# Optimization experiments

Measured on AMD Instinct MI355X. Metric: run time of the kernel, lower is better.

The kernel has to match this reference:

```python
import jax, jax.numpy as jnp
import numpy as np

MEMBRANE_DECAY = 0.95
REFRACTORY_PERIOD = 2.0


def setup_inputs() -> dict:
    key = jax.random.key(0)
    k0, k1, k2, k3 = jax.random.split(key, 4)
    B, S, I, H, O = 32, 1024, 256, 512, 256
    x = jax.random.normal(k0, (B, S, I), dtype=jnp.float32)
    input_weights = jax.random.normal(k1, (I, H), dtype=jnp.float32) * 0.1
    lateral_weights = jax.random.normal(k2, (H, H), dtype=jnp.float32) * 0.3
    output_weights = jax.random.normal(k3, (H, O), dtype=jnp.float32) * 0.1
    thresholds = jnp.ones((H,), dtype=jnp.float32)  # spike_threshold = 1.0
    return {"x": x, "input_weights": input_weights,
            "lateral_weights": lateral_weights,
            "output_weights": output_weights, "thresholds": thresholds}


def reference(x, input_weights, lateral_weights, output_weights, thresholds):
    # x: [B, S, I]. Precompute input currents for all timesteps: [B, S, H]
    inp_cur = jnp.einsum('bsi,ih->bsh', x, input_weights)
    B, S, H = inp_cur.shape
    dtype = x.dtype

    def step(carry, ic):
        mp, refrac, prev_spikes = carry  # each [B, H]
        # lateral feedback from previous timestep's spikes (zeros at t=0)
        lateral = prev_spikes @ lateral_weights
        mp = MEMBRANE_DECAY * mp + ic - lateral
        mp = jnp.where(refrac > 0, jnp.zeros((), dtype), mp)
        refrac = jnp.maximum(refrac - 1.0, 0.0)
        spikes = (mp >= thresholds).astype(dtype)
        mp = jnp.where(spikes > 0, jnp.zeros((), dtype), mp)
        refrac = jnp.where(spikes > 0, jnp.asarray(REFRACTORY_PERIOD, dtype), refrac)
        return (mp, refrac, spikes), spikes

    init = (jnp.zeros((B, H), dtype), jnp.zeros((B, H), dtype), jnp.zeros((B, H), dtype))
    _, spikes_seq = jax.lax.scan(step, init, jnp.swapaxes(inp_cur, 0, 1))  # [S, B, H]
    # output currents per timestep -> [B, S, O]
    return jnp.einsum('sbh,ho->bso', spikes_seq, output_weights)
```

## Files before the change

### kernel.cpp

```cpp
#include <hip/hip_runtime.h>
#include <stdint.h>


#define BB 32
#define SS 1024
#define II 256
#define HH 512
#define OO 256
#define NSPL 8
#define MAGICK 0x5A5A5A5A5A5A5A5AULL

#define TM 64
#define TN 64
#define TK 16

__global__ __launch_bounds__(256) void ic_gemm_f64(const float* __restrict__ x,
                                                   const float* __restrict__ win,
                                                   double* __restrict__ ic) {
    __shared__ float As[TK][TM + 4];
    __shared__ float Bs[TK][TN];
    const int tid = threadIdx.x;
    const int m0 = blockIdx.x * TM;
    const int n0 = blockIdx.y * TN;
    const int tx = tid & 15;
    const int ty = tid >> 4;

    double acc[4][4];
#pragma unroll
    for (int i = 0; i < 4; ++i)
#pragma unroll
        for (int j = 0; j < 4; ++j) acc[i][j] = 0.0;

    const int lr = tid >> 2;
    const int lq = tid & 3;
    const int br = tid >> 4;
    const int bq = tid & 15;

    for (int k0 = 0; k0 < II; k0 += TK) {
        float4 av = *(const float4*)(x + (size_t)(m0 + lr) * II + k0 + lq * 4);
        float4 bv = *(const float4*)(win + (size_t)(k0 + br) * HH + n0 + bq * 4);
        As[lq * 4 + 0][lr] = av.x;
        As[lq * 4 + 1][lr] = av.y;
        As[lq * 4 + 2][lr] = av.z;
        As[lq * 4 + 3][lr] = av.w;
        *(float4*)(&Bs[br][bq * 4]) = bv;
        __syncthreads();
#pragma unroll
        for (int kk = 0; kk < TK; ++kk) {
            float4 a = *(const float4*)(&As[kk][ty * 4]);
            float4 b = *(const float4*)(&Bs[kk][tx * 4]);
            const double a0 = (double)a.x, a1 = (double)a.y, a2 = (double)a.z, a3 = (double)a.w;
            const double b0 = (double)b.x, b1 = (double)b.y, b2 = (double)b.z, b3 = (double)b.w;
            acc[0][0] += a0 * b0; acc[0][1] += a0 * b1; acc[0][2] += a0 * b2; acc[0][3] += a0 * b3;
            acc[1][0] += a1 * b0; acc[1][1] += a1 * b1; acc[1][2] += a1 * b2; acc[1][3] += a1 * b3;
            acc[2][0] += a2 * b0; acc[2][1] += a2 * b1; acc[2][2] += a2 * b2; acc[2][3] += a2 * b3;
            acc[3][0] += a3 * b0; acc[3][1] += a3 * b1; acc[3][2] += a3 * b2; acc[3][3] += a3 * b3;
        }
        __syncthreads();
    }

#pragma unroll
    for (int i = 0; i < 4; ++i) {
        double* row = ic + (size_t)(m0 + ty * 4 + i) * HH + n0 + tx * 4;
#pragma unroll
        for (int j = 0; j < 4; ++j) row[j] = acc[i][j];
    }
}

__global__ __launch_bounds__(256) void snn_scan8(const double* __restrict__ ic,
                                                 const float* __restrict__ wlat,
                                                 const float* __restrict__ thr,
                                                 uint64_t* __restrict__ xq) {
    __shared__ int s_act[2][560];
    __shared__ int s_nact[2];
    __shared__ double s_part[16][68];
    __shared__ uint64_t s_m8[8];

    const int tid = threadIdx.x;
    const int bid = blockIdx.x;
    const int b = bid & 31;
    const int j = bid >> 5;
    const int ch = tid >> 4;
    const int qd = tid & 15;
    const int sw = (qd >> 2) & 3;

    const double* icb = ic + (size_t)b * SS * HH + (j << 6);
    uint64_t* xqb = xq + ((size_t)b * SS << 4);
    const char* wb = (const char*)wlat + (j << 8) + (qd << 4);

    const bool owner = (tid < 64);
    double mp = 0.0, th = 0.0, icv = 0.0;
    int refrac = 0, rsw = 0;
    if (owner) {
        th = (double)thr[(j << 6) + tid];
        rsw = tid ^ ((tid >> 4) & 3);
        icv = icb[tid];
    }
    if (tid == 0) { s_nact[0] = 0; s_nact[1] = 0; }
    for (int i = tid; i < 560; i += 256) { s_act[0][i] = 0; s_act[1][i] = 0; }
    __syncthreads();

    int cur = 0;
    for (int t = 0; t < SS; ++t) {
        const int nxt = cur ^ 1;

        const int n = s_nact[cur];
        const int* act = s_act[cur];
        const int kcnt = (n > ch) ? ((n - ch + 15) >> 4) : 0;

        double ac0 = 0.0, ac1 = 0.0, ac2 = 0.0, ac3 = 0.0;
        {
            int idx = ch;
            float4 f0 = *(const float4*)(wb + act[idx]);
            float4 f1 = *(const float4*)(wb + act[idx + 16]);
            for (int k = 0; k < kcnt; ++k) {
                float4 f2 = *(const float4*)(wb + act[idx + 32]);
                ac0 += (double)f0.x;
                ac1 += (double)f0.y;
                ac2 += (double)f0.z;
                ac3 += (double)f0.w;
                f0 = f1; f1 = f2; idx += 16;
            }
        }
        {
            const int pb = qd << 2;
            s_part[ch][(pb + 0) ^ sw] = ac0;
            s_part[ch][(pb + 1) ^ sw] = ac1;
            s_part[ch][(pb + 2) ^ sw] = ac2;
            s_part[ch][(pb + 3) ^ sw] = ac3;
        }
        __syncthreads();

        if (owner) {
            double l0 = 0.0, l1 = 0.0, l2 = 0.0, l3 = 0.0;
#pragma unroll
            for (int c = 0; c < 16; c += 4) {
                l0 += s_part[c + 0][rsw];
                l1 += s_part[c + 1][rsw];
                l2 += s_part[c + 2][rsw];
                l3 += s_part[c + 3][rsw];
            }
            const double lat = (l0 + l1) + (l2 + l3);
            mp = 0.95 * mp + icv - lat;
            if (refrac > 0) mp = 0.0;
            refrac = (refrac > 0) ? (refrac - 1) : 0;
            const bool spike = (mp >= th);
            if (spike) { mp = 0.0; refrac = 2; }

            const uint64_t bm = __ballot(spike);
            if (tid == 0) {
                uint64_t* cell = xqb + ((size_t)t << 4) + (j << 1);
                __hip_atomic_store(cell, bm, __ATOMIC_RELAXED,
                                   __HIP_MEMORY_SCOPE_AGENT);
                __hip_atomic_store(cell + 1, bm ^ MAGICK, __ATOMIC_RELAXED,
                                   __HIP_MEMORY_SCOPE_AGENT);
                s_m8[j] = bm;
            }

            if (tid < 16) {
                const int w = tid & 7;
                if (w != j) {
                    uint64_t* rc = xqb + ((size_t)t << 4) + (w << 1) + (tid >> 3);
                    long guard = 0;
                    uint64_t v;
                    for (;;) {
                        v = __hip_atomic_load(rc, __ATOMIC_RELAXED,
                                              __HIP_MEMORY_SCOPE_AGENT);
                        const uint64_t pv = __shfl(v, tid ^ 8, 64);
                        if ((v ^ pv) == MAGICK) break;
                        if (++guard > (1L << 31)) break;
                    }
                    if (tid < 8) s_m8[w] = v;
                }
            }
            icv = icb[(size_t)(t < SS - 1 ? t + 1 : t) * HH + tid];
        } else {
            for (int i = tid - 64; i < 560; i += 192) s_act[nxt][i] = 0;
        }
        __syncthreads();

        {
            int rr = tid;
#pragma unroll
            for (int pass = 0; pass < 2; ++pass, rr += 256) {
                const int w = rr >> 6, bit = rr & 63;
                int base = 0, tot = 0;
                uint64_t myw = 0;
#pragma unroll
                for (int u = 0; u < 8; ++u) {
                    const uint64_t mw = s_m8[u];
                    const int pc = __popcll(mw);
                    if (u < w) base += pc;
                    if (u == w) myw = mw;
                    tot += pc;
                }
                if ((myw >> bit) & 1ull)
                    s_act[nxt][base + __popcll(myw & ((1ull << bit) - 1ull))] =
                        rr << 11;
                if (tid == 0 && pass == 0) s_nact[nxt] = tot;
            }
        }
        __syncthreads();
        cur = nxt;
    }
}

__global__ __launch_bounds__(256) void out_gemm(const uint64_t* __restrict__ xq,
                                                const float* __restrict__ wout,
                                                float* __restrict__ out) {
    const int bt = blockIdx.x;
    const int o = threadIdx.x;
    __shared__ uint64_t sm[8];
    if (o < 8) sm[o] = xq[((size_t)bt << 4) + (o << 1)];
    __syncthreads();

    float acc = 0.0f;
#pragma unroll
    for (int w = 0; w < 8; ++w) {
        uint64_t bits = sm[w];
        while (bits) {
            const int h = (w << 6) + __ffsll((unsigned long long)bits) - 1;
            bits &= bits - 1;
            acc += wout[(size_t)h * OO + o];
        }
    }
    out[(size_t)bt * OO + o] = acc;
}

extern "C" void kernel_launch(void* const* d_in, const int* in_sizes, int n_in,
                              void* d_out, int out_size, void* d_ws, size_t ws_size,
                              hipStream_t stream) {
    const float* x    = (const float*)d_in[0];
    const float* win  = (const float*)d_in[1];
    const float* wlat = (const float*)d_in[2];
    const float* wout = (const float*)d_in[3];
    const float* thr  = (const float*)d_in[4];
    float* out = (float*)d_out;

    char* p = (char*)d_ws;
    double* ic = (double*)p;      p += (size_t)BB * SS * HH * sizeof(double);
    uint64_t* xq = (uint64_t*)p;

    const int M = BB * SS;
    ic_gemm_f64<<<dim3(M / TM, HH / TN), 256, 0, stream>>>(x, win, ic);
    snn_scan8<<<BB * NSPL, 256, 0, stream>>>(ic, wlat, thr, xq);
    out_gemm<<<M, 256, 0, stream>>>(xq, wout, out);
}
```

Measured before the change: 2.749 ms.

## Cache lateral weight slice in LDS and speed up cross-block spike exchange

Each scan block now copies its 512x64 slice of the lateral weights into shared memory, padded to 68 floats per row, and gathers active rows from LDS rather than global memory. The inter-block spike-mask exchange writes a second copy with sc0 stores and polls it with inline-asm sc0 loads, falling back to agent-scope atomics every eighth spin. The next-step input current load is moved ahead of the spin-wait. This targets per-timestep global latency on the serial scan, at the cost of about 139KB of LDS per block, non-portable inline assembly, and a shorter spin guard.

```diff
diff --git a/kernel.cpp b/kernel.cpp
--- a/kernel.cpp
+++ b/kernel.cpp
@@ -8,6 +8,7 @@
 #define HH 512
 #define OO 256
 #define NSPL 8
+#define SLW 68
 #define MAGICK 0x5A5A5A5A5A5A5A5AULL
 
 #define TM 64
@@ -67,10 +68,12 @@
     }
 }
 
-__global__ __launch_bounds__(256) void snn_scan8(const double* __restrict__ ic,
-                                                 const float* __restrict__ wlat,
-                                                 const float* __restrict__ thr,
-                                                 uint64_t* __restrict__ xq) {
+__global__ __launch_bounds__(256) void snn_scan8v2(const double* __restrict__ ic,
+                                                   const float* __restrict__ wlat,
+                                                   const float* __restrict__ thr,
+                                                   uint64_t* __restrict__ xf,
+                                                   uint64_t* __restrict__ xa) {
+    __shared__ float s_w[HH * SLW];
     __shared__ int s_act[2][560];
     __shared__ int s_nact[2];
     __shared__ double s_part[16][68];
@@ -85,8 +88,13 @@
     const int sw = (qd >> 2) & 3;
 
     const double* icb = ic + (size_t)b * SS * HH + (j << 6);
-    uint64_t* xqb = xq + ((size_t)b * SS << 4);
-    const char* wb = (const char*)wlat + (j << 8) + (qd << 4);
+    uint64_t* xfb = xf + ((size_t)b * SS << 4);
+    uint64_t* xab = xa + ((size_t)b * SS << 4);
+
+    for (int r = tid >> 4; r < HH; r += 16) {
+        const float4 v = *(const float4*)(wlat + (size_t)r * HH + (j << 6) + (qd << 2));
+        *(float4*)&s_w[r * SLW + (qd << 2)] = v;
+    }
 
     const bool owner = (tid < 64);
     double mp = 0.0, th = 0.0, icv = 0.0;
@@ -100,6 +108,8 @@
     for (int i = tid; i < 560; i += 256) { s_act[0][i] = 0; s_act[1][i] = 0; }
     __syncthreads();
 
+    const char* wb = (const char*)s_w + (qd << 4);
+
     int cur = 0;
     for (int t = 0; t < SS; ++t) {
         const int nxt = cur ^ 1;
@@ -111,15 +121,15 @@
         double ac0 = 0.0, ac1 = 0.0, ac2 = 0.0, ac3 = 0.0;
         {
             int idx = ch;
-            float4 f0 = *(const float4*)(wb + act[idx]);
-            float4 f1 = *(const float4*)(wb + act[idx + 16]);
+            int o0 = act[idx];
             for (int k = 0; k < kcnt; ++k) {
-                float4 f2 = *(const float4*)(wb + act[idx + 32]);
-                ac0 += (double)f0.x;
-                ac1 += (double)f0.y;
-                ac2 += (double)f0.z;
-                ac3 += (double)f0.w;
-                f0 = f1; f1 = f2; idx += 16;
+                const int o1 = act[idx + 16];
+                const float4 f = *(const float4*)(wb + o0);
+                ac0 += (double)f.x;
+                ac1 += (double)f.y;
+                ac2 += (double)f.z;
+                ac3 += (double)f.w;
+                o0 = o1; idx += 16;
             }
         }
         {
@@ -149,31 +159,46 @@
 
             const uint64_t bm = __ballot(spike);
             if (tid == 0) {
-                uint64_t* cell = xqb + ((size_t)t << 4) + (j << 1);
-                __hip_atomic_store(cell, bm, __ATOMIC_RELAXED,
+                uint64_t* fc = xfb + ((size_t)t << 4) + (j << 1);
+                uint64_t* ac_ = xab + ((size_t)t << 4) + (j << 1);
+                const uint64_t bmx = bm ^ MAGICK;
+                asm volatile("global_store_dwordx2 %0, %1, off sc0\n\t"
+                             "global_store_dwordx2 %0, %2, off offset:8 sc0"
+                             :: "v"(fc), "v"(bm), "v"(bmx) : "memory");
+                __hip_atomic_store(ac_, bm, __ATOMIC_RELAXED,
                                    __HIP_MEMORY_SCOPE_AGENT);
-                __hip_atomic_store(cell + 1, bm ^ MAGICK, __ATOMIC_RELAXED,
+                __hip_atomic_store(ac_ + 1, bmx, __ATOMIC_RELAXED,
                                    __HIP_MEMORY_SCOPE_AGENT);
                 s_m8[j] = bm;
             }
+            icv = icb[(size_t)(t < SS - 1 ? t + 1 : t) * HH + tid];
 
             if (tid < 16) {
                 const int w = tid & 7;
                 if (w != j) {
-                    uint64_t* rc = xqb + ((size_t)t << 4) + (w << 1) + (tid >> 3);
+                    const uint64_t* fw = xfb + ((size_t)t << 4) + (w << 1) + (tid >> 3);
+                    const uint64_t* aw = xab + ((size_t)t << 4) + (w << 1) + (tid >> 3);
+                    uint64_t v = 0;
                     long guard = 0;
-                    uint64_t v;
                     for (;;) {
-                        v = __hip_atomic_load(rc, __ATOMIC_RELAXED,
-                                              __HIP_MEMORY_SCOPE_AGENT);
-                        const uint64_t pv = __shfl(v, tid ^ 8, 64);
-                        if ((v ^ pv) == MAGICK) break;
-                        if (++guard > (1L << 31)) break;
+                        uint64_t f;
+                        asm volatile("global_load_dwordx2 %0, %1, off sc0\n\t"
+                                     "s_waitcnt vmcnt(0)"
+                                     : "=&v"(f) : "v"(fw) : "memory");
+                        const uint64_t pf = __shfl(f, tid ^ 8, 64);
+                        if ((f ^ pf) == MAGICK) { v = (tid < 8) ? f : pf; break; }
+                        ++guard;
+                        if ((guard & 7) == 0) {
+                            const uint64_t a = __hip_atomic_load(
+                                aw, __ATOMIC_RELAXED, __HIP_MEMORY_SCOPE_AGENT);
+                            const uint64_t pa = __shfl(a, tid ^ 8, 64);
+                            if ((a ^ pa) == MAGICK) { v = (tid < 8) ? a : pa; break; }
+                        }
+                        if (guard > (1L << 24)) break;
                     }
                     if (tid < 8) s_m8[w] = v;
                 }
             }
-            icv = icb[(size_t)(t < SS - 1 ? t + 1 : t) * HH + tid];
         } else {
             for (int i = tid - 64; i < 560; i += 192) s_act[nxt][i] = 0;
         }
@@ -196,7 +221,7 @@
                 }
                 if ((myw >> bit) & 1ull)
                     s_act[nxt][base + __popcll(myw & ((1ull << bit) - 1ull))] =
-                        rr << 11;
+                        rr * (SLW * 4);
                 if (tid == 0 && pass == 0) s_nact[nxt] = tot;
             }
         }
@@ -205,13 +230,13 @@
     }
 }
 
-__global__ __launch_bounds__(256) void out_gemm(const uint64_t* __restrict__ xq,
+__global__ __launch_bounds__(256) void out_gemm(const uint64_t* __restrict__ xa,
                                                 const float* __restrict__ wout,
                                                 float* __restrict__ out) {
     const int bt = blockIdx.x;
     const int o = threadIdx.x;
     __shared__ uint64_t sm[8];
-    if (o < 8) sm[o] = xq[((size_t)bt << 4) + (o << 1)];
+    if (o < 8) sm[o] = xa[((size_t)bt << 4) + (o << 1)];
     __syncthreads();
 
     float acc = 0.0f;
@@ -239,10 +264,11 @@
 
     char* p = (char*)d_ws;
     double* ic = (double*)p;      p += (size_t)BB * SS * HH * sizeof(double);
-    uint64_t* xq = (uint64_t*)p;
+    uint64_t* xa = (uint64_t*)p;  p += ((size_t)BB * SS << 4) * sizeof(uint64_t);
+    uint64_t* xf = (uint64_t*)p;
 
     const int M = BB * SS;
     ic_gemm_f64<<<dim3(M / TM, HH / TN), 256, 0, stream>>>(x, win, ic);
-    snn_scan8<<<BB * NSPL, 256, 0, stream>>>(ic, wlat, thr, xq);
-    out_gemm<<<M, 256, 0, stream>>>(xq, wout, out);
-}
+    snn_scan8v2<<<BB * NSPL, 256, 0, stream>>>(ic, wlat, thr, xf, xa);
+    out_gemm<<<M, 256, 0, stream>>>(xa, wout, out);
+}
```

Result: slower. 3.433 ms (+24.9%).
